# Kernel optimization log

Hardware: AMD Instinct MI355X
Metric: run time of the kernel (lower is better)

The kernel has to match this reference:

```python
import jax, jax.numpy as jnp
import numpy as np

B, S, D = 2, 2048, 2048
H = 32
HD = D // H  # 64
EPS = 1e-4


def setup_inputs() -> dict:
    key = jax.random.key(0)
    ks = jax.random.split(key, 9)
    hidden_states = jax.random.normal(ks[0], (B, S, D), dtype=jnp.float32)
    # multiplicative causal mask
    attention_mask = jnp.tril(jnp.ones((S, S), dtype=jnp.float32))[None, None]
    scale = 0.02
    wq = jax.random.normal(ks[1], (D, D), dtype=jnp.float32) * scale
    wk = jax.random.normal(ks[2], (D, D), dtype=jnp.float32) * scale
    wv = jax.random.normal(ks[3], (D, D), dtype=jnp.float32) * scale
    wo = jax.random.normal(ks[4], (D, D), dtype=jnp.float32) * scale
    bq = jax.random.normal(ks[5], (D,), dtype=jnp.float32) * scale
    bk = jax.random.normal(ks[6], (D,), dtype=jnp.float32) * scale
    bv = jax.random.normal(ks[7], (D,), dtype=jnp.float32) * scale
    bo = jax.random.normal(ks[8], (D,), dtype=jnp.float32) * scale
    return {"hidden_states": hidden_states, "attention_mask": attention_mask,
            "wq": wq, "bq": bq, "wk": wk, "bk": bk, "wv": wv, "bv": bv,
            "wo": wo, "bo": bo}


def _split_heads(x):
    # [B, S, D] -> [B, H, S, HD]
    b, s, _ = x.shape
    return x.reshape(b, s, H, HD).transpose(0, 2, 1, 3)


def reference(hidden_states, attention_mask, wq, bq, wk, bk, wv, bv, wo, bo):
    scaling = HD ** -0.5
    q = (hidden_states @ wq.T + bq) * scaling
    k = hidden_states @ wk.T + bk
    v = hidden_states @ wv.T + bv
    q, k, v = _split_heads(q), _split_heads(k), _split_heads(v)
    # ELU+1 feature map, then sum-normalize over head dim
    q = jax.nn.elu(q) + 1.0
    k = jax.nn.elu(k) + 1.0
    q = q / (q.sum(-1, keepdims=True) + EPS)
    k = k / (k.sum(-1, keepdims=True) + EPS)
    # quadratic attention: [B, H, S, S]
    attn = jnp.einsum('bhsd,bhtd->bhst', q, k) * (HD ** -0.5)
    attn = attn * attention_mask  # multiplicative mask
    out = jnp.einsum('bhst,bhtd->bhsd', attn, v)  # [B, H, S, HD]
    out = out.transpose(0, 2, 1, 3).reshape(hidden_states.shape[0], -1, D)
    return out @ wo.T + bo
```

## Files before the change

### kernel.cpp

```cpp
#include <hip/hip_runtime.h>

typedef __bf16 bf16x8 __attribute__((ext_vector_type(8)));
typedef float f32x4 __attribute__((ext_vector_type(4)));

#define GLDS(g, l) __builtin_amdgcn_global_load_lds(                              \
    (const __attribute__((address_space(1))) void*)(g),                            \
    (__attribute__((address_space(3))) void*)(l), 16, 0, 0)

__device__ __forceinline__ unsigned short f2bf(float f) {
  unsigned int u = __builtin_bit_cast(unsigned int, f);
  u = (u + 0x7fffu + ((u >> 16) & 1u)) >> 16;
  return (unsigned short)u;
}
__device__ __forceinline__ float bf2f(unsigned short h) {
  unsigned int u = ((unsigned int)h) << 16;
  return __builtin_bit_cast(float, u);
}

__global__ __launch_bounds__(256) void cvt_all(
    const float* __restrict__ hs, const float* __restrict__ w0,
    const float* __restrict__ w1, const float* __restrict__ w2,
    const float* __restrict__ w3, unsigned short* __restrict__ hs_bf,
    unsigned short* __restrict__ wall_bf) {
  const int i = blockIdx.x * 256 + threadIdx.x;
  const float* src;
  unsigned short* dst;
  int off;
  if (i < 2097152) { src = hs; dst = hs_bf; off = i; }
  else {
    const int j = i - 2097152;
    const int y = j >> 20;
    src = (y == 0) ? w0 : (y == 1) ? w1 : (y == 2) ? w2 : w3;
    dst = wall_bf + (size_t)y * 4194304;
    off = j & 1048575;
  }
  float4 v = ((const float4*)src)[off];
  ushort4 o;
  o.x = f2bf(v.x); o.y = f2bf(v.y); o.z = f2bf(v.z); o.w = f2bf(v.w);
  ((ushort4*)dst)[off] = o;
}

__global__ __launch_bounds__(512, 2) void gemm384_qkv(
    const unsigned short* __restrict__ A, const unsigned short* __restrict__ Bw,
    const float* __restrict__ bq, const float* __restrict__ bk, const float* __restrict__ bv,
    unsigned short* __restrict__ oQ, unsigned short* __restrict__ oK,
    unsigned short* __restrict__ oV) {
  constexpr int K = 2048, NT = 32;
  __shared__ unsigned short lds[81920];
  const int tid = threadIdx.x, lane = tid & 63, wid = tid >> 6;
  const int wm = wid >> 1, wn = wid & 1;

  const int g0 = blockIdx.x;
  const int wg = (g0 & 7) * 32 + (g0 >> 3);
  const int chunk = wg >> 5, l = wg & 31;
  const int bx = (chunk & 3) * 4 + (l >> 3);
  const int by = (chunk >> 2) * 8 + (l & 7);

  const int rloc = tid >> 3;
  const size_t gcoff = (size_t)(((lane & 7) ^ (lane >> 3)) << 3);
  const unsigned short* gA = A  + (size_t)(by * 256 + rloc) * K + gcoff;
  const unsigned short* gB = Bw + (size_t)(bx * 384 + rloc) * K + gcoff;

#define ABu(b) ((b) * 16384)
#define BBu(b) (32768 + (b) * 24576)
#define STAGE_A(c, b) GLDS(gA + (size_t)(c) * 64 * K, lds + ABu(b) + (c) * 4096 + wid * 512)
#define STAGE_B(c, b) GLDS(gB + (size_t)(c) * 64 * K, lds + BBu(b) + (c) * 4096 + wid * 512)

  const int arow = (wm * 64 + (lane & 15)) * 64;
  const int brow = (wn * 192 + (lane & 15)) * 64;
  const int sw0 = (((lane >> 4)) ^ (lane & 7)) << 3;
  const int sw1 = ((4 + (lane >> 4)) ^ (lane & 7)) << 3;

  f32x4 acc[4][12] = {};

  STAGE_A(0, 0); STAGE_A(1, 0); STAGE_A(2, 0); STAGE_A(3, 0);
  STAGE_B(0, 0); STAGE_B(1, 0); STAGE_B(2, 0); STAGE_B(3, 0); STAGE_B(4, 0); STAGE_B(5, 0);
  gA += 64; gB += 64;
  asm volatile("s_waitcnt vmcnt(0)" ::: "memory");
  __builtin_amdgcn_s_barrier();

  for (int t = 0; t < NT; ++t) {
    const int Ab = ABu(t & 1) + arow;
    const int Bb = BBu(t & 1) + brow;
    const int sb = (t + 1) & 1;
    const bool st = (t + 1 < NT);
    bf16x8 Af[4], Bf[6];

    if (st) { STAGE_B(0, sb); STAGE_B(1, sb); STAGE_B(2, sb); }
#pragma unroll
    for (int m = 0; m < 4; ++m) Af[m] = *(const bf16x8*)&lds[Ab + m * 1024 + sw0];
#pragma unroll
    for (int n = 0; n < 6; ++n) Bf[n] = *(const bf16x8*)&lds[Bb + n * 1024 + sw0];
    __builtin_amdgcn_s_barrier();
    __builtin_amdgcn_s_setprio(1);
#pragma unroll
    for (int m = 0; m < 4; ++m)
#pragma unroll
      for (int n = 0; n < 6; ++n)
        acc[m][n] = __builtin_amdgcn_mfma_f32_16x16x32_bf16(Af[m], Bf[n], acc[m][n], 0, 0, 0);
    __builtin_amdgcn_s_setprio(0);
    __builtin_amdgcn_s_barrier();

    if (st) { STAGE_B(3, sb); STAGE_B(4, sb); STAGE_B(5, sb); }
#pragma unroll
    for (int n = 0; n < 6; ++n) Bf[n] = *(const bf16x8*)&lds[Bb + (n + 6) * 1024 + sw0];
    __builtin_amdgcn_s_barrier();
    __builtin_amdgcn_s_setprio(1);
#pragma unroll
    for (int m = 0; m < 4; ++m)
#pragma unroll
      for (int n = 0; n < 6; ++n)
        acc[m][n + 6] = __builtin_amdgcn_mfma_f32_16x16x32_bf16(Af[m], Bf[n], acc[m][n + 6], 0, 0, 0);
    __builtin_amdgcn_s_setprio(0);
    __builtin_amdgcn_s_barrier();

    if (st) { STAGE_A(0, sb); STAGE_A(1, sb); STAGE_A(2, sb); STAGE_A(3, sb); }
#pragma unroll
    for (int m = 0; m < 4; ++m) Af[m] = *(const bf16x8*)&lds[Ab + m * 1024 + sw1];
#pragma unroll
    for (int n = 0; n < 6; ++n) Bf[n] = *(const bf16x8*)&lds[Bb + n * 1024 + sw1];
    __builtin_amdgcn_s_barrier();
    __builtin_amdgcn_s_setprio(1);
#pragma unroll
    for (int m = 0; m < 4; ++m)
#pragma unroll
      for (int n = 0; n < 6; ++n)
        acc[m][n] = __builtin_amdgcn_mfma_f32_16x16x32_bf16(Af[m], Bf[n], acc[m][n], 0, 0, 0);
    __builtin_amdgcn_s_setprio(0);
    __builtin_amdgcn_s_barrier();

#pragma unroll
    for (int n = 0; n < 6; ++n) Bf[n] = *(const bf16x8*)&lds[Bb + (n + 6) * 1024 + sw1];
    __builtin_amdgcn_s_barrier();
    __builtin_amdgcn_s_setprio(1);
#pragma unroll
    for (int m = 0; m < 4; ++m)
#pragma unroll
      for (int n = 0; n < 6; ++n)
        acc[m][n + 6] = __builtin_amdgcn_mfma_f32_16x16x32_bf16(Af[m], Bf[n], acc[m][n + 6], 0, 0, 0);
    __builtin_amdgcn_s_setprio(0);
    if (st) {
      gA += 64; gB += 64;
      asm volatile("s_waitcnt vmcnt(0)" ::: "memory");
    }
    __builtin_amdgcn_s_barrier();
  }

  const int head0 = bx * 6 + wn * 3;
#pragma unroll
  for (int g = 0; g < 3; ++g) {
    const int head = head0 + g;
    const int type = head >> 5;
    const int h = head & 31;
    const float* bias = (type == 0) ? bq : (type == 1) ? bk : bv;
    unsigned short* dst = (type == 0) ? oQ : (type == 1) ? oK : oV;
    float bv4[4];
#pragma unroll
    for (int j = 0; j < 4; ++j) bv4[j] = bias[h * 64 + j * 16 + (lane & 15)];
#pragma unroll
    for (int m = 0; m < 4; ++m) {
#pragma unroll
      for (int r = 0; r < 4; ++r) {
        const int row = by * 256 + wm * 64 + m * 16 + ((lane >> 4) << 2) + r;
        const int bb = row >> 11, s = row & 2047;
        float e[4];
        float loc = 0.f;
#pragma unroll
        for (int j = 0; j < 4; ++j) {
          float v = acc[m][g * 4 + j][r] + bv4[j];
          if (type == 0) v *= 0.125f;
          if (type < 2) v = (v > 0.f) ? (v + 1.f) : __expf(v);
          e[j] = v; loc += v;
        }
        if (type < 2) {
#pragma unroll
          for (int off = 1; off < 16; off <<= 1) loc += __shfl_xor(loc, off, 64);
          const float inv = 1.f / (loc + 1e-4f);
#pragma unroll
          for (int j = 0; j < 4; ++j) e[j] *= inv;
        }
        const size_t base = ((size_t)((bb << 5) + h) * 2048 + s) * 64;
#pragma unroll
        for (int j = 0; j < 4; ++j) dst[base + j * 16 + (lane & 15)] = f2bf(e[j]);
      }
    }
  }
#undef ABu
#undef BBu
#undef STAGE_A
#undef STAGE_B
}

__global__ __launch_bounds__(512, 2) void gemm128_wo(
    const unsigned short* __restrict__ A, const unsigned short* __restrict__ Bw,
    const float* __restrict__ b0, float* __restrict__ C) {
  constexpr int K = 2048, NT = 32;
  __shared__ unsigned short lds[73728];
  const int tid = threadIdx.x, lane = tid & 63, wid = tid >> 6;
  const int wm = wid >> 2, wn = wid & 3;

  const int g0 = blockIdx.x;
  const int wg = (g0 & 7) * 32 + (g0 >> 3);
  const int l = wg % 32;
  const int chunk = wg / 32;
  const int bx2 = (chunk % 4) * 2 + l / 16;
  const int by2 = (chunk / 4) * 16 + l % 16;

  const int rloc = wid * 8 + (lane >> 3);
  const size_t gcoff = (size_t)(((lane & 7) ^ (lane >> 3)) << 3);
  const unsigned short* gA[2];
  const unsigned short* gB[4];
#pragma unroll
  for (int c = 0; c < 2; ++c) gA[c] = A + (size_t)(by2 * 128 + c * 64 + rloc) * K + gcoff;
#pragma unroll
  for (int c = 0; c < 4; ++c) gB[c] = Bw + (size_t)(bx2 * 256 + c * 64 + rloc) * K + gcoff;

  int aoff[4][2], boff[4][2];
#pragma unroll
  for (int m = 0; m < 4; ++m)
#pragma unroll
    for (int kk = 0; kk < 2; ++kk) {
      aoff[m][kk] = (wm * 64 + m * 16 + (lane & 15)) * 64 +
                    ((((kk << 2) + (lane >> 4)) ^ (lane & 7)) << 3);
      boff[m][kk] = (wn * 64 + m * 16 + (lane & 15)) * 64 +
                    ((((kk << 2) + (lane >> 4)) ^ (lane & 7)) << 3);
    }

  f32x4 acc[4][4] = {};

#define AB(b) ((b) * 8192)
#define BB(b) (24576 + (b) * 16384)
#define STAGE_A(c, b) GLDS(gA[c], lds + AB(b) + (c) * 4096 + wid * 512)
#define STAGE_B(c, b) GLDS(gB[c], lds + BB(b) + (c) * 4096 + wid * 512)

  STAGE_A(0, 0); STAGE_A(1, 0); STAGE_B(0, 0); STAGE_B(1, 0); STAGE_B(2, 0); STAGE_B(3, 0);
#pragma unroll
  for (int c = 0; c < 2; ++c) gA[c] += 64;
#pragma unroll
  for (int c = 0; c < 4; ++c) gB[c] += 64;
  STAGE_A(0, 1); STAGE_A(1, 1); STAGE_B(0, 1); STAGE_B(1, 1); STAGE_B(2, 1); STAGE_B(3, 1);
#pragma unroll
  for (int c = 0; c < 2; ++c) gA[c] += 64;
#pragma unroll
  for (int c = 0; c < 4; ++c) gB[c] += 64;
  asm volatile("s_waitcnt vmcnt(6)" ::: "memory");
  __builtin_amdgcn_s_barrier();

  for (int t = 0; t < NT; ++t) {
    const int b = t % 3;
    const int sb = (t + 2) % 3;
    const bool doStage = (t + 2 < NT);

    if (doStage) { STAGE_A(0, sb); STAGE_A(1, sb); STAGE_B(0, sb); STAGE_B(1, sb); }
    bf16x8 af[4], bfr[4];
#pragma unroll
    for (int m = 0; m < 4; ++m) af[m] = *(const bf16x8*)&lds[AB(b) + aoff[m][0]];
#pragma unroll
    for (int n = 0; n < 4; ++n) bfr[n] = *(const bf16x8*)&lds[BB(b) + boff[n][0]];
    __builtin_amdgcn_s_barrier();
    __builtin_amdgcn_s_setprio(1);
#pragma unroll
    for (int m = 0; m < 4; ++m)
#pragma unroll
      for (int n = 0; n < 4; ++n)
        acc[m][n] = __builtin_amdgcn_mfma_f32_16x16x32_bf16(af[m], bfr[n], acc[m][n], 0, 0, 0);
    __builtin_amdgcn_s_setprio(0);
    __builtin_amdgcn_s_barrier();

    if (doStage) { STAGE_B(2, sb); STAGE_B(3, sb); }
#pragma unroll
    for (int c = 0; c < 2; ++c) gA[c] += 64;
#pragma unroll
    for (int c = 0; c < 4; ++c) gB[c] += 64;
#pragma unroll
    for (int m = 0; m < 4; ++m) af[m] = *(const bf16x8*)&lds[AB(b) + aoff[m][1]];
#pragma unroll
    for (int n = 0; n < 4; ++n) bfr[n] = *(const bf16x8*)&lds[BB(b) + boff[n][1]];
    __builtin_amdgcn_s_barrier();
    __builtin_amdgcn_s_setprio(1);
#pragma unroll
    for (int m = 0; m < 4; ++m)
#pragma unroll
      for (int n = 0; n < 4; ++n)
        acc[m][n] = __builtin_amdgcn_mfma_f32_16x16x32_bf16(af[m], bfr[n], acc[m][n], 0, 0, 0);
    __builtin_amdgcn_s_setprio(0);
    if (t < NT - 1) {
      if (doStage) asm volatile("s_waitcnt vmcnt(6)" ::: "memory");
      else         asm volatile("s_waitcnt vmcnt(0)" ::: "memory");
    }
    __builtin_amdgcn_s_barrier();
  }

#pragma unroll
  for (int n = 0; n < 4; ++n) {
    const int col = bx2 * 256 + wn * 64 + n * 16 + (lane & 15);
    const float bv_ = b0[col];
#pragma unroll
    for (int m = 0; m < 4; ++m) {
      const int row0 = by2 * 128 + wm * 64 + m * 16 + ((lane >> 4) << 2);
#pragma unroll
      for (int r = 0; r < 4; ++r)
        C[(size_t)(row0 + r) * 2048 + col] = acc[m][n][r] + bv_;
    }
  }
#undef AB
#undef BB
#undef STAGE_A
#undef STAGE_B
}

__global__ __launch_bounds__(256) void chunk_state(
    const unsigned short* __restrict__ Kn, const unsigned short* __restrict__ Vn,
    unsigned short* __restrict__ stT) {
  __shared__ unsigned short Kt[64 * 72];
  __shared__ unsigned short Vt[64 * 72];
  const int c = blockIdx.x, bh = blockIdx.y;
  const int tid = threadIdx.x, lane = tid & 63, wid = tid >> 6;
  const size_t base = (size_t)bh * 2048 * 64 + (size_t)c * 64 * 64;
#pragma unroll
  for (int i = 0; i < 16; ++i) {
    const int ii = i * 256 + tid;
    const int t = ii >> 6, d = ii & 63;
    Kt[d * 72 + t] = Kn[base + ii];
    Vt[d * 72 + t] = Vn[base + ii];
  }
  __syncthreads();
  f32x4 acc[4] = {};
#pragma unroll
  for (int ks = 0; ks < 2; ++ks) {
    const int ko = ks * 32 + (lane >> 4) * 8;
    bf16x8 a = *(const bf16x8*)&Vt[(wid * 16 + (lane & 15)) * 72 + ko];
#pragma unroll
    for (int ej = 0; ej < 4; ++ej) {
      bf16x8 bb = *(const bf16x8*)&Kt[(ej * 16 + (lane & 15)) * 72 + ko];
      acc[ej] = __builtin_amdgcn_mfma_f32_16x16x32_bf16(a, bb, acc[ej], 0, 0, 0);
    }
  }
  const size_t obase = ((size_t)bh * 32 + c) * 4096;
#pragma unroll
  for (int ej = 0; ej < 4; ++ej) {
    const int e = ej * 16 + (lane & 15);
    const int d0 = wid * 16 + ((lane >> 4) << 2);
#pragma unroll
    for (int r = 0; r < 4; ++r)
      stT[obase + (size_t)(d0 + r) * 64 + e] = f2bf(acc[ej][r]);
  }
}

__global__ __launch_bounds__(256) void prefix_state(
    const unsigned short* __restrict__ stT, unsigned short* __restrict__ cumT) {
  const int g = blockIdx.x * 256 + threadIdx.x;
  const int bh = g >> 12, e = g & 4095;
  float run = 0.f;
  for (int c = 0; c < 32; ++c) {
    const size_t idx = (((size_t)bh * 32 + c) << 12) + e;
    const float v = bf2f(stT[idx]);
    cumT[idx] = f2bf(run);
    run += v;
  }
}

__global__ __launch_bounds__(256) void attn_intra(
    const unsigned short* __restrict__ Qn, const unsigned short* __restrict__ Kn,
    const unsigned short* __restrict__ Vn, const unsigned short* __restrict__ cumT,
    unsigned short* __restrict__ aout) {
  __shared__ unsigned short Qs[64 * 72];
  __shared__ unsigned short Ks[64 * 72];
  __shared__ unsigned short Vt[64 * 72];
  __shared__ unsigned short St[64 * 72];
  __shared__ unsigned short Ps[64 * 72];
  const int c = blockIdx.x, bh = blockIdx.y;
  const int tid = threadIdx.x, lane = tid & 63, wid = tid >> 6;
  const size_t base = (size_t)bh * 2048 * 64 + (size_t)c * 64 * 64;
  const size_t sbase = ((size_t)bh * 32 + c) * 4096;
#pragma unroll
  for (int i = 0; i < 16; ++i) {
    const int ii = i * 256 + tid;
    const int t = ii >> 6, d = ii & 63;
    Qs[t * 72 + d] = Qn[base + ii];
    Ks[t * 72 + d] = Kn[base + ii];
    Vt[d * 72 + t] = Vn[base + ii];
    St[t * 72 + d] = cumT[sbase + ii];
  }
  __syncthreads();
  f32x4 sacc[4] = {};
#pragma unroll
  for (int ks = 0; ks < 2; ++ks) {
    const int ko = ks * 32 + (lane >> 4) * 8;
    bf16x8 a = *(const bf16x8*)&Qs[(wid * 16 + (lane & 15)) * 72 + ko];
#pragma unroll
    for (int tj = 0; tj < 4; ++tj) {
      bf16x8 bb = *(const bf16x8*)&Ks[(tj * 16 + (lane & 15)) * 72 + ko];
      sacc[tj] = __builtin_amdgcn_mfma_f32_16x16x32_bf16(a, bb, sacc[tj], 0, 0, 0);
    }
  }
#pragma unroll
  for (int tj = 0; tj < 4; ++tj) {
    const int t = tj * 16 + (lane & 15);
    const int s0 = wid * 16 + ((lane >> 4) << 2);
#pragma unroll
    for (int r = 0; r < 4; ++r) {
      const float v = (t <= s0 + r) ? sacc[tj][r] : 0.f;
      Ps[(s0 + r) * 72 + t] = f2bf(v);
    }
  }
  __syncthreads();
  f32x4 oacc[4] = {};
#pragma unroll
  for (int ks = 0; ks < 2; ++ks) {
    const int ko = ks * 32 + (lane >> 4) * 8;
    bf16x8 a = *(const bf16x8*)&Ps[(wid * 16 + (lane & 15)) * 72 + ko];
    bf16x8 a2 = *(const bf16x8*)&Qs[(wid * 16 + (lane & 15)) * 72 + ko];
#pragma unroll
    for (int dj = 0; dj < 4; ++dj) {
      bf16x8 bv_ = *(const bf16x8*)&Vt[(dj * 16 + (lane & 15)) * 72 + ko];
      oacc[dj] = __builtin_amdgcn_mfma_f32_16x16x32_bf16(a, bv_, oacc[dj], 0, 0, 0);
      bf16x8 bs_ = *(const bf16x8*)&St[(dj * 16 + (lane & 15)) * 72 + ko];
      oacc[dj] = __builtin_amdgcn_mfma_f32_16x16x32_bf16(a2, bs_, oacc[dj], 0, 0, 0);
    }
  }
  const int b = bh >> 5, h = bh & 31;
#pragma unroll
  for (int dj = 0; dj < 4; ++dj) {
    const int d = dj * 16 + (lane & 15);
    const int s0 = wid * 16 + ((lane >> 4) << 2);
#pragma unroll
    for (int r = 0; r < 4; ++r) {
      const size_t row = (size_t)(b * 2048 + c * 64 + s0 + r);
      aout[row * 2048 + h * 64 + d] = f2bf(0.125f * oacc[dj][r]);
    }
  }
}

extern "C" void kernel_launch(void* const* d_in, const int* in_sizes, int n_in,
                              void* d_out, int out_size, void* d_ws, size_t ws_size,
                              hipStream_t stream) {
  const float* hs = (const float*)d_in[0];
  const float* wq = (const float*)d_in[2];
  const float* bq = (const float*)d_in[3];
  const float* wk = (const float*)d_in[4];
  const float* bk = (const float*)d_in[5];
  const float* wv = (const float*)d_in[6];
  const float* bv = (const float*)d_in[7];
  const float* wo = (const float*)d_in[8];
  const float* bo = (const float*)d_in[9];
  float* out = (float*)d_out;
  char* ws = (char*)d_ws;

  unsigned short* hs_bf   = (unsigned short*)(ws);
  unsigned short* wall_bf = (unsigned short*)(ws + 16777216);
  unsigned short* Qn      = (unsigned short*)(ws + 50331648);
  unsigned short* Kn      = (unsigned short*)(ws + 67108864);
  unsigned short* Vn      = (unsigned short*)(ws + 83886080);
  unsigned short* stT     = (unsigned short*)(ws + 100663296);
  unsigned short* cumT    = (unsigned short*)(ws + 117440512);
  unsigned short* aout    = (unsigned short*)(ws + 134217728);

  cvt_all<<<24576, 256, 0, stream>>>(hs, wq, wk, wv, wo, hs_bf, wall_bf);

  gemm384_qkv<<<256, 512, 0, stream>>>(hs_bf, wall_bf, bq, bk, bv, Qn, Kn, Vn);

  chunk_state<<<dim3(32, 64), 256, 0, stream>>>(Kn, Vn, stT);
  prefix_state<<<1024, 256, 0, stream>>>(stT, cumT);
  attn_intra<<<dim3(32, 64), 256, 0, stream>>>(Qn, Kn, Vn, cumT, aout);

  gemm128_wo<<<256, 512, 0, stream>>>(aout, wall_bf + 12582912, bo, out);
}
```

Before: 197.7 us.

## Rework QKV GEMM to 256x256 tiles with finer-grained 8-phase LDS pipeline

Replaces the 256x384 QKV projection GEMM (256 blocks) with a 256x256 tile kernel launched on 384 blocks. LDS is split into half-tiles staged in an interleaved eight-phase schedule so global-to-LDS loads overlap MFMA work, and waits use partial vmcnt. Because a head's 64 columns now span two warps, the epilogue exchanges per-row partial sums through LDS with extra block syncs. The aim is better CU coverage and lower LDS use per block, at the cost of more barriers and a more complex epilogue.

Result: slower. 235.3 us (+19.0%).

```diff
diff --git a/kernel.cpp b/kernel.cpp
--- a/kernel.cpp
+++ b/kernel.cpp
@@ -40,155 +40,191 @@
   ((ushort4*)dst)[off] = o;
 }
 
-__global__ __launch_bounds__(512, 2) void gemm384_qkv(
+__global__ __launch_bounds__(512, 2) void gemm256_qkv(
     const unsigned short* __restrict__ A, const unsigned short* __restrict__ Bw,
     const float* __restrict__ bq, const float* __restrict__ bk, const float* __restrict__ bv,
     unsigned short* __restrict__ oQ, unsigned short* __restrict__ oK,
     unsigned short* __restrict__ oV) {
-  constexpr int K = 2048, NT = 32;
-  __shared__ unsigned short lds[81920];
+  constexpr int K = 2048;
+  __shared__ unsigned short lds[65536];
   const int tid = threadIdx.x, lane = tid & 63, wid = tid >> 6;
-  const int wm = wid >> 1, wn = wid & 1;
+  const int wm = wid >> 2;
+  const int wn = wid & 3;
+  const int l15 = lane & 15;
 
   const int g0 = blockIdx.x;
-  const int wg = (g0 & 7) * 32 + (g0 >> 3);
-  const int chunk = wg >> 5, l = wg & 31;
-  const int bx = (chunk & 3) * 4 + (l >> 3);
-  const int by = (chunk >> 2) * 8 + (l & 7);
-
-  const int rloc = tid >> 3;
-  const size_t gcoff = (size_t)(((lane & 7) ^ (lane >> 3)) << 3);
-  const unsigned short* gA = A  + (size_t)(by * 256 + rloc) * K + gcoff;
-  const unsigned short* gB = Bw + (size_t)(bx * 384 + rloc) * K + gcoff;
-
-#define ABu(b) ((b) * 16384)
-#define BBu(b) (32768 + (b) * 24576)
-#define STAGE_A(c, b) GLDS(gA + (size_t)(c) * 64 * K, lds + ABu(b) + (c) * 4096 + wid * 512)
-#define STAGE_B(c, b) GLDS(gB + (size_t)(c) * 64 * K, lds + BBu(b) + (c) * 4096 + wid * 512)
-
-  const int arow = (wm * 64 + (lane & 15)) * 64;
-  const int brow = (wn * 192 + (lane & 15)) * 64;
+  const int wg = (g0 & 7) * 48 + (g0 >> 3);
+  const int bx = wg / 16;
+  const int by = wg % 16;
+
+  const int srow = tid >> 3;
+  const size_t gsw = (size_t)(((lane & 7) ^ (srow & 7)) << 3);
+  const unsigned short* gA = A  + (size_t)(by * 256 + srow) * K + gsw;
+  const unsigned short* gB = Bw + (size_t)(bx * 256 + srow) * K + gsw;
+
+#define STAGE_A(b, h, tt)                                                                    \
+  do {                                                                                       \
+    GLDS(gA + (size_t)((h) * 128) * K + (size_t)(tt) * 64,                                   \
+         lds + ((b) * 2 + (h)) * 8192 + wid * 512);                                          \
+    GLDS(gA + (size_t)((h) * 128 + 64) * K + (size_t)(tt) * 64,                              \
+         lds + ((b) * 2 + (h)) * 8192 + 4096 + wid * 512);                                   \
+  } while (0)
+#define STAGE_B(b, h, tt)                                                                    \
+  do {                                                                                       \
+    GLDS(gB + (size_t)((h) * 128) * K + (size_t)(tt) * 64,                                   \
+         lds + 32768 + ((b) * 2 + (h)) * 8192 + wid * 512);                                  \
+    GLDS(gB + (size_t)((h) * 128 + 64) * K + (size_t)(tt) * 64,                              \
+         lds + 32768 + ((b) * 2 + (h)) * 8192 + 4096 + wid * 512);                           \
+  } while (0)
+
   const int sw0 = (((lane >> 4)) ^ (lane & 7)) << 3;
   const int sw1 = ((4 + (lane >> 4)) ^ (lane & 7)) << 3;
-
-  f32x4 acc[4][12] = {};
-
-  STAGE_A(0, 0); STAGE_A(1, 0); STAGE_A(2, 0); STAGE_A(3, 0);
-  STAGE_B(0, 0); STAGE_B(1, 0); STAGE_B(2, 0); STAGE_B(3, 0); STAGE_B(4, 0); STAGE_B(5, 0);
-  gA += 64; gB += 64;
-  asm volatile("s_waitcnt vmcnt(0)" ::: "memory");
+  const int aro = (wm * 64 + l15) * 64;
+  const int bro = (wn * 32 + l15) * 64;
+
+  f32x4 acc[8][4] = {};
+  bf16x8 Af[8], Bf[4];
+
+#define PH_CORE(BUF, MH, NH, LA, LB)                                                         \
+  do {                                                                                       \
+    if (LA) {                                                                                \
+      const int ab_ = ((BUF) * 2 + (MH)) * 8192 + aro;                                       \
+      _Pragma("unroll") for (int mq = 0; mq < 4; ++mq) {                                     \
+        Af[mq * 2]     = *(const bf16x8*)&lds[ab_ + mq * 1024 + sw0];                        \
+        Af[mq * 2 + 1] = *(const bf16x8*)&lds[ab_ + mq * 1024 + sw1];                        \
+      }                                                                                      \
+    }                                                                                        \
+    if (LB) {                                                                                \
+      const int bb_ = 32768 + ((BUF) * 2 + (NH)) * 8192 + bro;                               \
+      _Pragma("unroll") for (int nq = 0; nq < 2; ++nq) {                                     \
+        Bf[nq * 2]     = *(const bf16x8*)&lds[bb_ + nq * 1024 + sw0];                        \
+        Bf[nq * 2 + 1] = *(const bf16x8*)&lds[bb_ + nq * 1024 + sw1];                        \
+      }                                                                                      \
+    }                                                                                        \
+    __builtin_amdgcn_sched_barrier(0);                                                       \
+    __builtin_amdgcn_s_barrier();                                                            \
+    asm volatile("s_waitcnt lgkmcnt(0)" ::: "memory");                                       \
+    __builtin_amdgcn_sched_barrier(0);                                                       \
+    __builtin_amdgcn_s_setprio(1);                                                           \
+    _Pragma("unroll") for (int mq = 0; mq < 4; ++mq)                                         \
+      _Pragma("unroll") for (int nq = 0; nq < 2; ++nq)                                       \
+        _Pragma("unroll") for (int kk = 0; kk < 2; ++kk)                                     \
+          acc[(MH) * 4 + mq][(NH) * 2 + nq] = __builtin_amdgcn_mfma_f32_16x16x32_bf16(       \
+              Af[mq * 2 + kk], Bf[nq * 2 + kk], acc[(MH) * 4 + mq][(NH) * 2 + nq], 0, 0, 0); \
+    __builtin_amdgcn_s_setprio(0);                                                           \
+  } while (0)
+
+  STAGE_A(0, 0, 0); STAGE_A(0, 1, 0); STAGE_B(0, 0, 0); STAGE_B(0, 1, 0);
+  STAGE_B(1, 0, 1); STAGE_A(1, 1, 1);
+  asm volatile("s_waitcnt vmcnt(4)" ::: "memory");
   __builtin_amdgcn_s_barrier();
 
-  for (int t = 0; t < NT; ++t) {
-    const int Ab = ABu(t & 1) + arow;
-    const int Bb = BBu(t & 1) + brow;
-    const int sb = (t + 1) & 1;
-    const bool st = (t + 1 < NT);
-    bf16x8 Af[4], Bf[6];
-
-    if (st) { STAGE_B(0, sb); STAGE_B(1, sb); STAGE_B(2, sb); }
-#pragma unroll
-    for (int m = 0; m < 4; ++m) Af[m] = *(const bf16x8*)&lds[Ab + m * 1024 + sw0];
-#pragma unroll
-    for (int n = 0; n < 6; ++n) Bf[n] = *(const bf16x8*)&lds[Bb + n * 1024 + sw0];
-    __builtin_amdgcn_s_barrier();
-    __builtin_amdgcn_s_setprio(1);
-#pragma unroll
-    for (int m = 0; m < 4; ++m)
-#pragma unroll
-      for (int n = 0; n < 6; ++n)
-        acc[m][n] = __builtin_amdgcn_mfma_f32_16x16x32_bf16(Af[m], Bf[n], acc[m][n], 0, 0, 0);
-    __builtin_amdgcn_s_setprio(0);
-    __builtin_amdgcn_s_barrier();
-
-    if (st) { STAGE_B(3, sb); STAGE_B(4, sb); STAGE_B(5, sb); }
-#pragma unroll
-    for (int n = 0; n < 6; ++n) Bf[n] = *(const bf16x8*)&lds[Bb + (n + 6) * 1024 + sw0];
-    __builtin_amdgcn_s_barrier();
-    __builtin_amdgcn_s_setprio(1);
-#pragma unroll
-    for (int m = 0; m < 4; ++m)
-#pragma unroll
-      for (int n = 0; n < 6; ++n)
-        acc[m][n + 6] = __builtin_amdgcn_mfma_f32_16x16x32_bf16(Af[m], Bf[n], acc[m][n + 6], 0, 0, 0);
-    __builtin_amdgcn_s_setprio(0);
-    __builtin_amdgcn_s_barrier();
-
-    if (st) { STAGE_A(0, sb); STAGE_A(1, sb); STAGE_A(2, sb); STAGE_A(3, sb); }
-#pragma unroll
-    for (int m = 0; m < 4; ++m) Af[m] = *(const bf16x8*)&lds[Ab + m * 1024 + sw1];
-#pragma unroll
-    for (int n = 0; n < 6; ++n) Bf[n] = *(const bf16x8*)&lds[Bb + n * 1024 + sw1];
-    __builtin_amdgcn_s_barrier();
-    __builtin_amdgcn_s_setprio(1);
-#pragma unroll
-    for (int m = 0; m < 4; ++m)
-#pragma unroll
-      for (int n = 0; n < 6; ++n)
-        acc[m][n] = __builtin_amdgcn_mfma_f32_16x16x32_bf16(Af[m], Bf[n], acc[m][n], 0, 0, 0);
-    __builtin_amdgcn_s_setprio(0);
-    __builtin_amdgcn_s_barrier();
-
-#pragma unroll
-    for (int n = 0; n < 6; ++n) Bf[n] = *(const bf16x8*)&lds[Bb + (n + 6) * 1024 + sw1];
-    __builtin_amdgcn_s_barrier();
-    __builtin_amdgcn_s_setprio(1);
-#pragma unroll
-    for (int m = 0; m < 4; ++m)
-#pragma unroll
-      for (int n = 0; n < 6; ++n)
-        acc[m][n + 6] = __builtin_amdgcn_mfma_f32_16x16x32_bf16(Af[m], Bf[n], acc[m][n + 6], 0, 0, 0);
-    __builtin_amdgcn_s_setprio(0);
-    if (st) {
-      gA += 64; gB += 64;
-      asm volatile("s_waitcnt vmcnt(0)" ::: "memory");
-    }
-    __builtin_amdgcn_s_barrier();
-  }
-
-  const int head0 = bx * 6 + wn * 3;
-#pragma unroll
-  for (int g = 0; g < 3; ++g) {
-    const int head = head0 + g;
-    const int type = head >> 5;
-    const int h = head & 31;
+  for (int g = 0; g < 16; ++g) {
+    const bool full = (g < 15);
+    const int t0 = 2 * g;
+
+    STAGE_B(1, 1, t0 + 1);
+    PH_CORE(0, 0, 0, 1, 1);
+    __builtin_amdgcn_s_barrier();
+
+    STAGE_A(1, 0, t0 + 1);
+    PH_CORE(0, 1, 0, 1, 0);
+    __builtin_amdgcn_s_barrier();
+
+    if (full) STAGE_B(0, 0, t0 + 2);
+    PH_CORE(0, 1, 1, 0, 1);
+    __builtin_amdgcn_s_barrier();
+
+    if (full) STAGE_A(0, 1, t0 + 2);
+    PH_CORE(0, 0, 1, 1, 0);
+    if (full) asm volatile("s_waitcnt vmcnt(4)" ::: "memory");
+    else      asm volatile("s_waitcnt vmcnt(0)" ::: "memory");
+    __builtin_amdgcn_s_barrier();
+
+    if (full) STAGE_B(0, 1, t0 + 2);
+    PH_CORE(1, 0, 0, 1, 1);
+    __builtin_amdgcn_s_barrier();
+
+    if (full) STAGE_A(0, 0, t0 + 2);
+    PH_CORE(1, 1, 0, 1, 0);
+    __builtin_amdgcn_s_barrier();
+
+    if (full) STAGE_B(1, 0, t0 + 3);
+    PH_CORE(1, 1, 1, 0, 1);
+    __builtin_amdgcn_s_barrier();
+
+    if (full) STAGE_A(1, 1, t0 + 3);
+    PH_CORE(1, 0, 1, 1, 0);
+    if (full) asm volatile("s_waitcnt vmcnt(4)" ::: "memory");
+    __builtin_amdgcn_s_barrier();
+  }
+
+  float* tab = (float*)lds;
+  const int rsub = (lane >> 4) << 2;
+  const int hp = wn >> 1, strip = wn & 1;
+#pragma unroll
+  for (int nh = 0; nh < 2; ++nh) {
+    const int headg = bx * 4 + nh * 2 + hp;
+    const int type = headg >> 5;
+    const int h = headg & 31;
     const float* bias = (type == 0) ? bq : (type == 1) ? bk : bv;
     unsigned short* dst = (type == 0) ? oQ : (type == 1) ? oK : oV;
-    float bv4[4];
-#pragma unroll
-    for (int j = 0; j < 4; ++j) bv4[j] = bias[h * 64 + j * 16 + (lane & 15)];
-#pragma unroll
-    for (int m = 0; m < 4; ++m) {
-#pragma unroll
-      for (int r = 0; r < 4; ++r) {
-        const int row = by * 256 + wm * 64 + m * 16 + ((lane >> 4) << 2) + r;
-        const int bb = row >> 11, s = row & 2047;
-        float e[4];
-        float loc = 0.f;
-#pragma unroll
-        for (int j = 0; j < 4; ++j) {
-          float v = acc[m][g * 4 + j][r] + bv4[j];
-          if (type == 0) v *= 0.125f;
-          if (type < 2) v = (v > 0.f) ? (v + 1.f) : __expf(v);
-          e[j] = v; loc += v;
+    float bv2[2];
+#pragma unroll
+    for (int nq = 0; nq < 2; ++nq) bv2[nq] = bias[h * 64 + strip * 32 + nq * 16 + l15];
+#pragma unroll
+    for (int mh = 0; mh < 2; ++mh) {
+      float ev[4][2][4];
+      float ss[4][4];
+#pragma unroll
+      for (int mq = 0; mq < 4; ++mq)
+#pragma unroll
+        for (int r = 0; r < 4; ++r) {
+          float s_ = 0.f;
+#pragma unroll
+          for (int nq = 0; nq < 2; ++nq) {
+            float v = acc[mh * 4 + mq][nh * 2 + nq][r] + bv2[nq];
+            if (type == 0) v *= 0.125f;
+            if (type < 2) v = (v > 0.f) ? (v + 1.f) : __expf(v);
+            ev[mq][nq][r] = v; s_ += v;
+          }
+#pragma unroll
+          for (int off = 1; off < 16; off <<= 1) s_ += __shfl_xor(s_, off, 64);
+          ss[mq][r] = s_;
         }
-        if (type < 2) {
-#pragma unroll
-          for (int off = 1; off < 16; off <<= 1) loc += __shfl_xor(loc, off, 64);
-          const float inv = 1.f / (loc + 1e-4f);
-#pragma unroll
-          for (int j = 0; j < 4; ++j) e[j] *= inv;
+      const int tbase = ((wm * 2 + hp) * 2 + strip) * 64;
+      if (type < 2 && (lane & 15) == 0) {
+#pragma unroll
+        for (int mq = 0; mq < 4; ++mq)
+#pragma unroll
+          for (int r = 0; r < 4; ++r)
+            tab[tbase + mq * 16 + rsub + r] = ss[mq][r];
+      }
+      __syncthreads();
+      const int pbase = ((wm * 2 + hp) * 2 + (strip ^ 1)) * 64;
+#pragma unroll
+      for (int mq = 0; mq < 4; ++mq) {
+#pragma unroll
+        for (int r = 0; r < 4; ++r) {
+          float inv = 1.f;
+          if (type < 2) {
+            const float tot = ss[mq][r] + tab[pbase + mq * 16 + rsub + r];
+            inv = 1.f / (tot + 1e-4f);
+          }
+          const int row = by * 256 + mh * 128 + wm * 64 + mq * 16 + rsub + r;
+          const int bb = row >> 11, sx = row & 2047;
+          const size_t obase = ((size_t)((bb << 5) + h) * 2048 + sx) * 64 + strip * 32;
+#pragma unroll
+          for (int nq = 0; nq < 2; ++nq)
+            dst[obase + nq * 16 + l15] = f2bf(ev[mq][nq][r] * inv);
         }
-        const size_t base = ((size_t)((bb << 5) + h) * 2048 + s) * 64;
-#pragma unroll
-        for (int j = 0; j < 4; ++j) dst[base + j * 16 + (lane & 15)] = f2bf(e[j]);
       }
-    }
-  }
-#undef ABu
-#undef BBu
+      __syncthreads();
+    }
+  }
 #undef STAGE_A
 #undef STAGE_B
+#undef PH_CORE
 }
 
 __global__ __launch_bounds__(512, 2) void gemm128_wo(
@@ -458,7 +494,7 @@
 
   cvt_all<<<24576, 256, 0, stream>>>(hs, wq, wk, wv, wo, hs_bf, wall_bf);
 
-  gemm384_qkv<<<256, 512, 0, stream>>>(hs_bf, wall_bf, bq, bk, bv, Qn, Kn, Vn);
+  gemm256_qkv<<<384, 512, 0, stream>>>(hs_bf, wall_bf, bq, bk, bv, Qn, Kn, Vn);
 
   chunk_state<<<dim3(32, 64), 256, 0, stream>>>(Kn, Vn, stT);
   prefix_state<<<1024, 256, 0, stream>>>(stT, cumT);
```
